# Optimization experiments

Hardware: AMD Instinct MI355X
Metric: run time of the kernel (lower is better)

Reference implementation:

```python
import jax, jax.numpy as jnp
import numpy as np
from jax.scipy.special import logsumexp

# ---- problem sizes ----
N, M, D, K = 3072, 3072, 64, 8
# geomloss SamplesLoss('sinkhorn', p=2, blur=0.05, scaling=0.8): cost = |x-y|^2 / 2
BLUR = 0.05
EPS = BLUR ** 2          # final entropic temperature = blur^p
SCAL2 = 0.8 ** 2         # eps annealing factor per iteration = scaling^p
NITER = 30               # fixed-length eps-scaling schedule (jit-friendly)


def _sqdist(x, y):
    # squared euclidean pairwise distances [n, m]
    return (x * x).sum(-1)[:, None] + (y * y).sum(-1)[None, :] - 2.0 * (x @ y.T)


def setup_inputs() -> dict:
    rng = np.random.default_rng(0)
    true_c = 3.0 * rng.normal(size=(K, D)).astype(np.float32)
    lab_t = rng.integers(0, K, size=M)
    target = (true_c[lab_t] + rng.normal(size=(M, D))).astype(np.float32)
    lab_x = rng.integers(0, K, size=N)
    x = (true_c[lab_x] + rng.normal(size=(N, D))).astype(np.float32)
    # Lloyd kmeans on target (emulates kmeans() in LossKMeans.__init__, no_grad precompute)
    C = target[rng.choice(M, K, replace=False)].copy()
    for _ in range(20):
        d = ((target[:, None, :] - C[None, :, :]) ** 2).sum(-1)
        assign = d.argmin(1)
        for k in range(K):
            m = assign == k
            if m.any():
                C[k] = target[m].mean(0)
    d = ((target[:, None, :] - C[None, :, :]) ** 2).sum(-1)
    pred_t = d.argmin(1).astype(np.int32)
    # approx_cluster_filling: soft-assignment fractions per cluster
    s = -d
    s = s - s.max(1, keepdims=True)
    e = np.exp(s)
    soft = e / e.sum(1, keepdims=True)
    filling_target = (soft.sum(0) / M).astype(np.float32)
    return {
        "x": jnp.asarray(x),
        "target": jnp.asarray(target),
        "cluster_centers": jnp.asarray(C.astype(np.float32)),
        "filling_target": jnp.asarray(filling_target),
        "prediction_target": jnp.asarray(pred_t),
    }


def _sinkhorn_potentials(C, loga, logb):
    # log-domain Sinkhorn with geometric eps annealing, run on a detached cost
    eps0 = jnp.maximum(jnp.max(C), EPS)
    f0 = jnp.zeros(C.shape[0], C.dtype)
    g0 = jnp.zeros(C.shape[1], C.dtype)

    def body(carry, t):
        f, g = carry
        eps = jnp.maximum(eps0 * (SCAL2 ** t), EPS)
        f = -eps * logsumexp(logb[None, :] + (g[None, :] - C) / eps, axis=1)
        g = -eps * logsumexp(loga[:, None] + (f[:, None] - C) / eps, axis=0)
        return (f, g), None

    (f, g), _ = jax.lax.scan(body, (f0, g0), jnp.arange(NITER, dtype=C.dtype))
    return f, g


def _ot(C, loga, logb, a, b):
    # geomloss-style gradient: iterate with stopped grads, one final differentiable update
    f, g = _sinkhorn_potentials(jax.lax.stop_gradient(C), loga, logb)
    f = jax.lax.stop_gradient(f)
    g = jax.lax.stop_gradient(g)
    f2 = -EPS * logsumexp(logb[None, :] + (g[None, :] - C) / EPS, axis=1)
    g2 = -EPS * logsumexp(loga[:, None] + (f[:, None] - C) / EPS, axis=0)
    return jnp.sum(a * f2) + jnp.sum(b * g2)


def _weights(mask, n):
    cnt = mask.sum()
    a = jnp.where(mask, 1.0 / jnp.maximum(cnt, 1).astype(jnp.float32), 0.0)
    a = jnp.where(cnt > 0, a, jnp.full(mask.shape, 1.0 / n, jnp.float32))  # safe fallback for empty cluster
    loga = jnp.where(a > 0, jnp.log(jnp.maximum(a, 1e-38)), -jnp.inf)
    return a, loga, cnt


def _forward(x, target, cluster_centers, filling_target, prediction_target):
    # loss_fil = compute_cluster_filling_mse(x, centers, filling_target)
    d_x = _sqdist(x, cluster_centers)                       # [N, K]
    filling_x = jax.nn.softmax(-d_x, axis=1).sum(0) / x.shape[0]
    loss_fil = jnp.mean((filling_x - filling_target) ** 2)
    # kmeans_predict
    pred_x = jnp.argmin(d_x, axis=1)
    # shared cost matrices (p=2 -> |x-y|^2 / 2), reused across the cluster loop
    Cxy = 0.5 * _sqdist(x, target)
    Cxx = 0.5 * _sqdist(x, x)
    Cyy = 0.5 * _sqdist(target, target)
    loss_med = jnp.float32(0.0)
    for k in range(K):  # fixed small loop over clusters (torch.unique loop, mask-guarded)
        mx = pred_x == k
        my = prediction_target == k
        a, loga, cx = _weights(mx, x.shape[0])
        b, logb, cy = _weights(my, target.shape[0])
        # debiased sinkhorn divergence (geomloss default debias=True)
        s = (_ot(Cxy, loga, logb, a, b)
             - 0.5 * _ot(Cxx, loga, loga, a, a)
             - 0.5 * _ot(Cyy, logb, logb, b, b))
        valid = ((cx > 0) & (cy > 0)).astype(jnp.float32)
        loss_med = loss_med + valid * s
    return loss_fil + loss_med


_fwd_jit = jax.jit(_forward)


def reference(x, target, cluster_centers, filling_target, prediction_target):
    return _fwd_jit(x, target, cluster_centers, filling_target, prediction_target)
```

## Files before the change

kernel.cpp:

```cpp
#include <hip/hip_runtime.h>
#include <hip/hip_bf16.h>
#include <float.h>

#define NN 3072
#define MM 3072
#define DD 64
#define KK 8
#define NPROB 24
#define NBLK 480

constexpr float C_EPS   = 0.0025f;
constexpr int   C_NITER = 30;
constexpr float LOG2E = 1.4426950408889634f;
constexpr float LN2F  = 0.6931471805599453f;
constexpr float L2_SCAL2 = -0.6438561897747247f;

__device__ __forceinline__ float ex2(float x){ return __builtin_amdgcn_exp2f(x); }
__device__ __forceinline__ float lg2(float x){ return __builtin_amdgcn_logf(x); }

__device__ __forceinline__ void  sst(float* p, float v){
    __hip_atomic_store(p, v, __ATOMIC_RELAXED, __HIP_MEMORY_SCOPE_SYSTEM);
}
__device__ __forceinline__ float sld(const float* p){
    return __hip_atomic_load((float*)p, __ATOMIC_RELAXED, __HIP_MEMORY_SCOPE_SYSTEM);
}

#define U_FILL 0
#define U_MAXC 8
#define U_CNTX 12
#define U_CNTY 20
#define U_POSX 28
#define U_POSY 36
#define U_OFFX 44
#define U_OFFY 53
#define U_PNX  64
#define U_PNY  88
#define U_PRB  112
#define U_PCB  136
#define U_PRS  160
#define U_PCS  184
#define U_PCOFF 208
#define U_PTOF  233
#define U_TOFF  257
#define U_ACCF  288
#define U_ACCG  312
#define U_TPPA  336
#define U_ASGN  384
#define U_BAR   896
#define U_XSQ  2432
#define U_YSQ  5504
#define U_PRED 8576
#define U_ROWS 11648
#define U_COLS 14720
#define U_FPOT 17792
#define U_GPOT 91520
#define U_SUBC 165248

__global__ __launch_bounds__(256) void k_prep(const float* __restrict__ x,
                                              const float* __restrict__ y,
                                              const float* __restrict__ cc,
                                              const int* __restrict__ predt,
                                              float* wf, int* wi) {
    int tid = threadIdx.x;
    if (blockIdx.x < 12) {
        __shared__ __align__(16) float c_s[KK][DD];
        __shared__ float csq_s[KK];
        __shared__ float fpart[KK];
        for (int e = tid; e < KK*DD; e += 256) c_s[e>>6][e&63] = cc[e];
        if (tid < KK) fpart[tid] = 0.f;
        __syncthreads();
        if (tid < KK) { float s=0.f; for (int d=0; d<DD; ++d){ float v=c_s[tid][d]; s+=v*v; } csq_s[tid]=s; }
        __syncthreads();
        int i = blockIdx.x*256 + tid;
        if (i < NN) {
            const float4* xr = (const float4*)(x + (size_t)i*DD);
            float4 xv[16];
            float xs = 0.f;
            #pragma unroll
            for (int q=0;q<16;++q){ xv[q]=xr[q];
                xs += xv[q].x*xv[q].x + xv[q].y*xv[q].y + xv[q].z*xv[q].z + xv[q].w*xv[q].w; }
            float dk[KK];
            #pragma unroll
            for (int k=0;k<KK;++k){
                const float4* cr = (const float4*)(&c_s[k][0]);
                float dot=0.f;
                #pragma unroll
                for (int q=0;q<16;++q){ float4 cv=cr[q];
                    dot += xv[q].x*cv.x + xv[q].y*cv.y + xv[q].z*cv.z + xv[q].w*cv.w; }
                dk[k] = xs + csq_s[k] - 2.f*dot;
            }
            float dmin = dk[0]; int am=0;
            #pragma unroll
            for (int k=1;k<KK;++k){ if (dk[k] < dmin){ dmin=dk[k]; am=k; } }
            float se=0.f; float ek[KK];
            #pragma unroll
            for (int k=0;k<KK;++k){ ek[k] = ex2((dmin-dk[k])*LOG2E); se+=ek[k]; }
            float inv = 1.f/se;
            #pragma unroll
            for (int k=0;k<KK;++k) atomicAdd(&fpart[k], ek[k]*inv);
            wf[U_XSQ + i] = xs;
            wi[U_PRED + i] = am;
            atomicAdd(&wi[U_CNTX + am], 1);
        }
        __syncthreads();
        if (tid < KK) atomicAdd(&wf[U_FILL + tid], fpart[tid]);
    } else {
        int j = (blockIdx.x-12)*256 + tid;
        if (j < MM) {
            const float4* yr = (const float4*)(y + (size_t)j*DD);
            float s=0.f;
            #pragma unroll
            for (int q=0;q<16;++q){ float4 v=yr[q]; s += v.x*v.x+v.y*v.y+v.z*v.z+v.w*v.w; }
            wf[U_YSQ + j] = s;
            atomicAdd(&wi[U_CNTY + predt[j]], 1);
        }
    }
}

__global__ void k_offsets(const float* __restrict__ ftarg, float* wf, int* wi, float* out) {
    if (threadIdx.x != 0) return;
    int offx=0, offy=0;
    wi[U_OFFX]=0; wi[U_OFFY]=0;
    for (int k=0;k<KK;++k){
        offx += wi[U_CNTX+k]; wi[U_OFFX+k+1]=offx;
        offy += wi[U_CNTY+k]; wi[U_OFFY+k+1]=offy;
    }
    int co=0, to=0;
    for (int k=0;k<KK;++k){
        int cx=wi[U_CNTX+k], cy=wi[U_CNTY+k];
        bool val = (cx>0)&&(cy>0);
        for (int t=0;t<3;++t){
            int p=k*3+t;
            int nx = val ? (t==2?cy:cx) : 0;
            int ny = val ? (t==1?cx:cy) : 0;
            wi[U_PNX+p]=nx; wi[U_PNY+p]=ny;
            wi[U_PRB+p] = (t==2)? wi[U_OFFY+k] : wi[U_OFFX+k];
            wi[U_PCB+p] = (t==1)? wi[U_OFFX+k] : wi[U_OFFY+k];
            wi[U_PRS+p] = (t==2)?1:0;
            wi[U_PCS+p] = (t==1)?0:1;
            wi[U_PCOFF+p]=co; co += nx*ny;
            wi[U_TOFF+p]=to; to += ((nx+31)>>5)*((ny+31)>>5);
            wf[U_ACCF+p]=0.f; wf[U_ACCG+p]=0.f;
        }
    }
    wi[U_PCOFF+NPROB]=co; wi[U_TOFF+NPROB]=to;
    int cto = co;
    for (int p=0;p<NPROB;++p){
        if (p%3 == 0){ wi[U_PTOF+p] = cto; cto += wi[U_PNX+p]*wi[U_PNY+p]; }
        else         { wi[U_PTOF+p] = wi[U_PCOFF+p]; }
    }
    long long wsum = 0;
    int wk[NPROB], quota[NPROB], done[NPROB];
    for (int p=0;p<NPROB;++p){
        int nx=wi[U_PNX+p], ny=wi[U_PNY+p];
        wk[p] = (nx>0 && ny>0) ? nx*ny : 0;
        wsum += wk[p];
    }
    if (wsum == 0){
        for (int b=0;b<NBLK;++b) wi[U_ASGN+b] = (0xFF<<16);
        for (int p=0;p<NPROB;++p) wi[U_TPPA+p] = 0;
    } else {
        int tot=0;
        for (int p=0;p<NPROB;++p){
            quota[p] = (wk[p]>0) ? (int)(((long long)NBLK*wk[p])/wsum) : 0;
            if (wk[p]>0 && quota[p]<1) quota[p]=1;
            tot += quota[p];
        }
        while (tot < NBLK){
            int best=-1; float br=-1.f;
            for (int p=0;p<NPROB;++p) if (wk[p]>0){
                float r = (float)wk[p]/(float)quota[p];
                if (r>br){br=r;best=p;}
            }
            quota[best]++; tot++;
        }
        while (tot > NBLK){
            int best=-1; float br=3.4e38f;
            for (int p=0;p<NPROB;++p) if (quota[p]>1){
                float r = (float)wk[p]/(float)(quota[p]-1);
                if (r<br){br=r;best=p;}
            }
            if (best<0) break;
            quota[best]--; tot--;
        }
        for (int p=0;p<NPROB;++p){ done[p]=0; wi[U_TPPA+p]=quota[p]; }
        int asg=0;
        while (asg < NBLK){
            for (int p=0;p<NPROB && asg<NBLK;++p)
                if (done[p] < quota[p]){ wi[U_ASGN+asg] = (p<<16)|done[p]; done[p]++; asg++; }
        }
    }
    float lf=0.f;
    for (int k=0;k<KK;++k){ float fx = wf[U_FILL+k]/(float)NN; float dd = fx - ftarg[k]; lf += dd*dd; }
    out[0] = lf/(float)KK;
}

__global__ __launch_bounds__(256) void k_scatter(const int* __restrict__ predt, int* wi) {
    int b = blockIdx.x;
    if (b < 12) {
        int i = b*256 + threadIdx.x;
        if (i < NN){ int k = wi[U_PRED+i]; int p = atomicAdd(&wi[U_POSX+k],1);
                     wi[U_ROWS + wi[U_OFFX+k] + p] = i; }
    } else {
        int j = (b-12)*256 + threadIdx.x;
        if (j < MM){ int k = predt[j]; int p = atomicAdd(&wi[U_POSY+k],1);
                     wi[U_COLS + wi[U_OFFY+k] + p] = j; }
    }
}

__global__ __launch_bounds__(256) void k_maxmat(const float* __restrict__ x,
                                                const float* __restrict__ y,
                                                float* wf, int* wi) {
    int z = blockIdx.z;
    const float* A = (z==2)? y : x;
    const float* B = (z==0)? y : ((z==1)? x : y);
    int aqo = (z==2)? U_YSQ : U_XSQ;
    int bqo = (z==1)? U_XSQ : U_YSQ;
    __shared__ float la[64][65];
    __shared__ float lb[64][65];
    __shared__ float laq[64], lbq[64];
    __shared__ float wred[4];
    int tid = threadIdx.x;
    int i0 = blockIdx.y*64, j0 = blockIdx.x*64;
    #pragma unroll
    for (int q=0;q<4;++q){
        int idx4 = tid + q*256;
        int r = idx4>>4; int c = (idx4&15)<<2;
        float4 va = *(const float4*)(A + (size_t)(i0+r)*DD + c);
        la[r][c]=va.x; la[r][c+1]=va.y; la[r][c+2]=va.z; la[r][c+3]=va.w;
        float4 vb = *(const float4*)(B + (size_t)(j0+r)*DD + c);
        lb[r][c]=vb.x; lb[r][c+1]=vb.y; lb[r][c+2]=vb.z; lb[r][c+3]=vb.w;
    }
    if (tid < 64) { laq[tid]=wf[aqo+i0+tid]; lbq[tid]=wf[bqo+j0+tid]; }
    __syncthreads();
    int r0 = (tid>>4)<<2, c0 = (tid&15)<<2;
    float acc[4][4] = {};
    for (int d=0; d<DD; ++d){
        float av[4], bv[4];
        #pragma unroll
        for (int a=0;a<4;++a){ av[a]=la[r0+a][d]; bv[a]=lb[c0+a][d]; }
        #pragma unroll
        for (int a=0;a<4;++a)
            #pragma unroll
            for (int b2=0;b2<4;++b2) acc[a][b2] += av[a]*bv[b2];
    }
    float m = 0.f;
    #pragma unroll
    for (int a=0;a<4;++a)
        #pragma unroll
        for (int b2=0;b2<4;++b2){
            float cst = 0.5f*(laq[r0+a]+lbq[c0+b2]) - acc[a][b2];
            m = fmaxf(m, cst);
        }
    #pragma unroll
    for (int o=32;o;o>>=1) m = fmaxf(m, __shfl_xor(m,o));
    int wid = tid>>6;
    if ((tid&63)==0) wred[wid]=m;
    __syncthreads();
    if (tid==0){
        float mm = fmaxf(fmaxf(wred[0],wred[1]),fmaxf(wred[2],wred[3]));
        atomicMax((unsigned int*)&wi[U_MAXC+z], __float_as_uint(mm));
    }
}

__global__ __launch_bounds__(256) void k_gather(const float* __restrict__ x,
                                                const float* __restrict__ y,
                                                float* wf, int* wi) {
    __shared__ float xs_[32][65], ys_[32][65];
    __shared__ float cs_[32][33];
    __shared__ float rq[32], cq[32];
    __shared__ int toff_s[NPROB+1];
    int tid = threadIdx.x;
    if (tid <= NPROB) toff_s[tid] = wi[U_TOFF+tid];
    __syncthreads();
    int total = toff_s[NPROB];
    for (int tix = blockIdx.x; tix < total; tix += gridDim.x){
        int p = 0;
        while (toff_s[p+1] <= tix) ++p;
        int nx = wi[U_PNX+p], ny = wi[U_PNY+p];
        int tpr = (ny+31)>>5;
        int loc = tix - toff_s[p];
        int i0 = (loc/tpr)<<5, j0 = (loc%tpr)<<5;
        int rbase = wi[U_PRB+p], cbase = wi[U_PCB+p];
        int rs = wi[U_PRS+p], cs = wi[U_PCS+p];
        const float* rsrc = rs? y : x;
        const float* csrc = cs? y : x;
        const int* rlist = wi + (rs? U_COLS : U_ROWS);
        const int* clist = wi + (cs? U_COLS : U_ROWS);
        int rqo = rs? U_YSQ : U_XSQ;
        int cqo = cs? U_YSQ : U_XSQ;
        size_t coff = (size_t)wi[U_PCOFF+p];
        #pragma unroll
        for (int q=0;q<2;++q){
            int idx4 = tid + q*256;
            int r = idx4>>4, c = (idx4&15)<<2;
            if (i0 + r < nx){
                int gi = rlist[rbase + i0 + r];
                float4 v = *(const float4*)(rsrc + (size_t)gi*DD + c);
                xs_[r][c]=v.x; xs_[r][c+1]=v.y; xs_[r][c+2]=v.z; xs_[r][c+3]=v.w;
                if (c==0) rq[r] = wf[rqo + gi];
            }
            if (j0 + r < ny){
                int gj = clist[cbase + j0 + r];
                float4 v = *(const float4*)(csrc + (size_t)gj*DD + c);
                ys_[r][c]=v.x; ys_[r][c+1]=v.y; ys_[r][c+2]=v.z; ys_[r][c+3]=v.w;
                if (c==0) cq[r] = wf[cqo + gj];
            }
        }
        __syncthreads();
        int r = tid>>3, cb = (tid&7)<<2;
        float cv[4] = {0.f,0.f,0.f,0.f};
        if (i0 + r < nx){
            float acc[4] = {0.f,0.f,0.f,0.f};
            for (int d=0; d<DD; ++d){
                float xv = xs_[r][d];
                #pragma unroll
                for (int q=0;q<4;++q) acc[q] += xv*ys_[cb+q][d];
            }
            float* dst = wf + U_SUBC + coff + (size_t)(i0+r)*ny + j0;
            #pragma unroll
            for (int q=0;q<4;++q){
                int j = cb+q;
                cv[q] = 0.5f*(rq[r]+cq[j]) - acc[q];
                if (j0 + j < ny) dst[j] = cv[q];
            }
        }
        if (p%3 == 0){
            #pragma unroll
            for (int q=0;q<4;++q) cs_[r][cb+q] = cv[q];
            __syncthreads();
            if (j0 + r < ny){
                float* dT = wf + U_SUBC + (size_t)wi[U_PTOF+p] + (size_t)(j0+r)*nx + i0;
                #pragma unroll
                for (int q=0;q<4;++q){
                    int ii = cb+q;
                    if (i0 + ii < nx) dT[ii] = cs_[ii][r];
                }
            }
        }
        __syncthreads();
    }
}

#define LD8F(JB, D00,D01,D02,D03,D10,D11,D12,D13, G0,G1,G2,G3) { \
    int ja=(JB)+lane; \
    D00=R0[ja]; D01=R0[ja+64]; D02=R0[ja+128]; D03=R0[ja+192]; \
    D10=R1[ja]; D11=R1[ja+64]; D12=R1[ja+128]; D13=R1[ja+192]; \
    G0=gs[ja];  G1=gs[ja+64];  G2=gs[ja+128];  G3=gs[ja+192]; }

#define PROCF(D0,D1,D2,D3, G0,G1,G2,G3, M, S) { \
    float t0=fmaf(D0,nie2,G0), t1=fmaf(D1,nie2,G1), t2=fmaf(D2,nie2,G2), t3=fmaf(D3,nie2,G3); \
    float cm = fmaxf(fmaxf(t0,t1),fmaxf(t2,t3)); \
    float mn = fmaxf(M, cm); \
    float sm = ex2(t0-mn) + ex2(t1-mn) + ex2(t2-mn) + ex2(t3-mn); \
    S = fmaf(S, ex2(M-mn), sm); \
    M = mn; }

#define LD8C(JB, D00,D01,D02,D03,D10,D11,D12,D13, G0,G1,G2,G3) { \
    int ja=(JB)+lane, jb_=(JB)+lane+64, jc=(JB)+lane+128, jd=(JB)+lane+192; \
    D00 = (ja <ncols)? R0[ja]  : 0.f;  D01 = (jb_<ncols)? R0[jb_] : 0.f; \
    D02 = (jc <ncols)? R0[jc]  : 0.f;  D03 = (jd <ncols)? R0[jd]  : 0.f; \
    D10 = (ja <ncols)? R1[ja]  : 0.f;  D11 = (jb_<ncols)? R1[jb_] : 0.f; \
    D12 = (jc <ncols)? R1[jc]  : 0.f;  D13 = (jd <ncols)? R1[jd]  : 0.f; \
    G0  = (ja <ncols)? gs[ja]  : 0.f;  G1  = (jb_<ncols)? gs[jb_] : 0.f; \
    G2  = (jc <ncols)? gs[jc]  : 0.f;  G3  = (jd <ncols)? gs[jd]  : 0.f; }

#define PROCR(JB, D0,D1,D2,D3, G0,G1,G2,G3, M, S) { \
    int ja=(JB)+lane, jb_=(JB)+lane+64, jc=(JB)+lane+128, jd=(JB)+lane+192; \
    float t0 = (ja <ncols)? fmaf(D0, nie2, G0) : -3e38f; \
    float t1 = (jb_<ncols)? fmaf(D1, nie2, G1) : -3e38f; \
    float t2 = (jc <ncols)? fmaf(D2, nie2, G2) : -3e38f; \
    float t3 = (jd <ncols)? fmaf(D3, nie2, G3) : -3e38f; \
    float cm = fmaxf(fmaxf(t0,t1),fmaxf(t2,t3)); \
    float mn = fmaxf(M, cm); \
    float sm = ex2(t0-mn) + ex2(t1-mn) + ex2(t2-mn) + ex2(t3-mn); \
    S = fmaf(S, ex2(M-mn), sm); \
    M = mn; }

template<bool FIN>
__device__ __forceinline__ void sweep(const float* __restrict__ Cb, int ldc, int nrows, int ncols,
                                      const float* __restrict__ gs, float* __restrict__ pot,
                                      float ie2, float neL, float l2n, int w, int lane,
                                      float* saccSlot)
{
    float nie2 = -ie2;
    float acc = 0.f;
    int nfull = ncols >> 8;
    int rem   = ncols & 255;
    for (int i0 = w*2; i0 < nrows; i0 += 16){
        int ia = i0;
        bool v1 = (i0+1 < nrows);
        int ib = v1 ? i0+1 : i0;
        const float* R0 = Cb + (size_t)ia*ldc;
        const float* R1 = Cb + (size_t)ib*ldc;
        float m0=-3e38f, m1=-3e38f, S0=0.f, S1=0.f;
        if (nfull){
            float a00,a01,a02,a03,a10,a11,a12,a13, ga0,ga1,ga2,ga3;
            LD8F(0, a00,a01,a02,a03,a10,a11,a12,a13, ga0,ga1,ga2,ga3)
            for (int v=1; v<nfull; ++v){
                float b00,b01,b02,b03,b10,b11,b12,b13, gb0,gb1,gb2,gb3;
                LD8F(v<<8, b00,b01,b02,b03,b10,b11,b12,b13, gb0,gb1,gb2,gb3)
                PROCF(a00,a01,a02,a03, ga0,ga1,ga2,ga3, m0, S0)
                PROCF(a10,a11,a12,a13, ga0,ga1,ga2,ga3, m1, S1)
                a00=b00; a01=b01; a02=b02; a03=b03;
                a10=b10; a11=b11; a12=b12; a13=b13;
                ga0=gb0; ga1=gb1; ga2=gb2; ga3=gb3;
            }
            PROCF(a00,a01,a02,a03, ga0,ga1,ga2,ga3, m0, S0)
            PROCF(a10,a11,a12,a13, ga0,ga1,ga2,ga3, m1, S1)
        }
        if (rem){
            int jb = nfull<<8;
            float c00,c01,c02,c03,c10,c11,c12,c13, gc0,gc1,gc2,gc3;
            LD8C(jb, c00,c01,c02,c03,c10,c11,c12,c13, gc0,gc1,gc2,gc3)
            PROCR(jb, c00,c01,c02,c03, gc0,gc1,gc2,gc3, m0, S0)
            PROCR(jb, c10,c11,c12,c13, gc0,gc1,gc2,gc3, m1, S1)
        }
        #pragma unroll
        for (int o=32;o;o>>=1){
            float mo=__shfl_xor(m0,o), So=__shfl_xor(S0,o);
            float mn=fmaxf(m0,mo); S0=fmaf(S0,ex2(m0-mn),So*ex2(mo-mn)); m0=mn;
            mo=__shfl_xor(m1,o); So=__shfl_xor(S1,o);
            mn=fmaxf(m1,mo); S1=fmaf(S1,ex2(m1-mn),So*ex2(mo-mn)); m1=mn;
        }
        if (lane==0){
            float v0  = neL*(m0 + lg2(S0) - l2n);
            float v1v = neL*(m1 + lg2(S1) - l2n);
            if (FIN){
                acc += v0;
                if (v1) acc += v1v;
            } else {
                sst(&pot[ia], v0);
                if (v1) sst(&pot[ib], v1v);
            }
        }
    }
    if (FIN && lane==0 && acc != 0.f) atomicAdd(saccSlot, acc);
}

__device__ __forceinline__ void tbar(int* cnt, int* gen, int tpp){
    __syncthreads();
    if (threadIdx.x == 0){
        asm volatile("s_waitcnt vmcnt(0)" ::: "memory");
        int g0 = __hip_atomic_load(gen, __ATOMIC_RELAXED, __HIP_MEMORY_SCOPE_AGENT);
        int a  = __hip_atomic_fetch_add(cnt, 1, __ATOMIC_RELAXED, __HIP_MEMORY_SCOPE_AGENT);
        if (a == tpp-1){
            __hip_atomic_store(cnt, 0, __ATOMIC_RELAXED, __HIP_MEMORY_SCOPE_AGENT);
            __hip_atomic_fetch_add(gen, 1, __ATOMIC_RELAXED, __HIP_MEMORY_SCOPE_AGENT);
        } else {
            int spins = 0;
            while (__hip_atomic_load(gen, __ATOMIC_RELAXED, __HIP_MEMORY_SCOPE_AGENT) == g0){
                __builtin_amdgcn_s_sleep(2);
                if (++spins > 200000) break;
            }
        }
    }
    __syncthreads();
}

__global__ __launch_bounds__(512) void k_sink(float* wf, int* wi, float* out) {
    int av = wi[U_ASGN + blockIdx.x];
    int p  = av>>16, sb = av & 0xFFFF;
    if (p >= NPROB) return;
    int nx = wi[U_PNX+p], ny = wi[U_PNY+p];
    if (nx <= 0 || ny <= 0) return;
    int tpp = wi[U_TPPA+p];
    int tid = threadIdx.x, w = tid>>6, lane = tid&63;
    float eps0 = fmaxf(__uint_as_float((unsigned)wi[U_MAXC + (p%3)]), C_EPS);
    const float* C  = wf + U_SUBC + (size_t)wi[U_PCOFF+p];
    const float* CT = wf + U_SUBC + (size_t)wi[U_PTOF+p];
    float* f = wf + U_FPOT + p*3072;
    float* g = wf + U_GPOT + p*3072;
    float l2ny = lg2((float)ny), l2nx = lg2((float)nx);
    int* cnt = wi + U_BAR + p*64;
    int* gen = cnt + 32;
    int rb0 = (sb*nx)/tpp, re0 = ((sb+1)*nx)/tpp;
    int cb0 = (sb*ny)/tpp, ce0 = ((sb+1)*ny)/tpp;
    __shared__ float gs[3072];

    for (int it=0; it<C_NITER; ++it){
        float eps = fmaxf(eps0*ex2((float)it*L2_SCAL2), C_EPS);
        float ie2 = LOG2E/eps, neL = -eps*LN2F;
        for (int j=tid; j<ny; j+=512) gs[j] = sld(g+j)*ie2;
        __syncthreads();
        sweep<false>(C + (size_t)rb0*ny, ny, re0-rb0, ny, gs, f+rb0, ie2, neL, l2ny, w, lane, nullptr);
        tbar(cnt, gen, tpp);
        for (int i=tid; i<nx; i+=512) gs[i] = sld(f+i)*ie2;
        __syncthreads();
        sweep<false>(CT + (size_t)cb0*nx, nx, ce0-cb0, nx, gs, g+cb0, ie2, neL, l2nx, w, lane, nullptr);
        tbar(cnt, gen, tpp);
    }
    {
        float ie2 = LOG2E/C_EPS, neL = -C_EPS*LN2F;
        for (int j=tid; j<ny; j+=512) gs[j] = sld(g+j)*ie2;
        __syncthreads();
        sweep<true>(C + (size_t)rb0*ny, ny, re0-rb0, ny, gs, nullptr, ie2, neL, l2ny, w, lane, &wf[U_ACCF+p]);
        __syncthreads();
        for (int i=tid; i<nx; i+=512) gs[i] = sld(f+i)*ie2;
        __syncthreads();
        sweep<true>(CT + (size_t)cb0*nx, nx, ce0-cb0, nx, gs, nullptr, ie2, neL, l2nx, w, lane, &wf[U_ACCG+p]);
    }
}

__global__ void k_final(float* wf, int* wi, float* out) {
    if (threadIdx.x != 0 || blockIdx.x != 0) return;
    float s = 0.f;
    for (int p=0; p<NPROB; ++p){
        int nx = wi[U_PNX+p], ny = wi[U_PNY+p];
        if (nx<=0 || ny<=0) continue;
        float wgt = (p%3==0) ? 1.f : -0.5f;
        s += wgt * (wf[U_ACCF+p]/(float)nx + wf[U_ACCG+p]/(float)ny);
    }
    out[0] += s;
}

extern "C" void kernel_launch(void* const* d_in, const int* in_sizes, int n_in,
                              void* d_out, int out_size, void* d_ws, size_t ws_size,
                              hipStream_t stream) {
    const float* x     = (const float*)d_in[0];
    const float* y     = (const float*)d_in[1];
    const float* cc    = (const float*)d_in[2];
    const float* ft    = (const float*)d_in[3];
    const int*   predt = (const int*)d_in[4];
    float* out = (float*)d_out;
    float* wf = (float*)d_ws;
    int*   wi = (int*)d_ws;

    hipMemsetAsync(d_ws, 0, 44*sizeof(int), stream);
    hipMemsetAsync(wi + U_BAR, 0, 24*64*sizeof(int), stream);
    hipMemsetAsync(wf + U_GPOT, 0, NPROB*3072*sizeof(float), stream);

    k_prep<<<24, 256, 0, stream>>>(x, y, cc, predt, wf, wi);
    k_offsets<<<1, 64, 0, stream>>>(ft, wf, wi, out);
    k_scatter<<<24, 256, 0, stream>>>(predt, wi);
    k_maxmat<<<dim3(48,48,3), 256, 0, stream>>>(x, y, wf, wi);
    k_gather<<<1024, 256, 0, stream>>>(x, y, wf, wi);

    k_sink<<<NBLK, 512, 0, stream>>>(wf, wi, out);
    k_final<<<1, 64, 0, stream>>>(wf, wi, out);
}
```

Measured before the change: 738.8 us.

## Enlarge maxmat tiles, skip symmetric blocks, and rebalance sweep rows per wave

The max-cost kernel now uses 128x128 tiles with an 8x8 register microtile, and skips lower-triangle blocks for the symmetric Cxx and Cyy matrices. This cuts global loads and the number of blocks. The Sinkhorn sweep now gives each wave a contiguous slice of rows computed globally across all blocks of a problem, and processes four rows per pass instead of two. That raises memory-level parallelism and balances work between waves, at the cost of more registers per thread and uneven slices when row counts are small.

```diff
diff --git a/kernel.cpp b/kernel.cpp
--- a/kernel.cpp
+++ b/kernel.cpp
@@ -212,46 +212,56 @@
                                                 const float* __restrict__ y,
                                                 float* wf, int* wi) {
     int z = blockIdx.z;
+    if (z && blockIdx.y > blockIdx.x) return;
     const float* A = (z==2)? y : x;
     const float* B = (z==0)? y : ((z==1)? x : y);
     int aqo = (z==2)? U_YSQ : U_XSQ;
     int bqo = (z==1)? U_XSQ : U_YSQ;
-    __shared__ float la[64][65];
-    __shared__ float lb[64][65];
-    __shared__ float laq[64], lbq[64];
+    __shared__ float la[128][65];
+    __shared__ float lb[128][65];
+    __shared__ float laq[128], lbq[128];
     __shared__ float wred[4];
     int tid = threadIdx.x;
-    int i0 = blockIdx.y*64, j0 = blockIdx.x*64;
+    int i0 = blockIdx.y*128, j0 = blockIdx.x*128;
     #pragma unroll
-    for (int q=0;q<4;++q){
-        int idx4 = tid + q*256;
-        int r = idx4>>4; int c = (idx4&15)<<2;
-        float4 va = *(const float4*)(A + (size_t)(i0+r)*DD + c);
-        la[r][c]=va.x; la[r][c+1]=va.y; la[r][c+2]=va.z; la[r][c+3]=va.w;
-        float4 vb = *(const float4*)(B + (size_t)(j0+r)*DD + c);
-        lb[r][c]=vb.x; lb[r][c+1]=vb.y; lb[r][c+2]=vb.z; lb[r][c+3]=vb.w;
-    }
-    if (tid < 64) { laq[tid]=wf[aqo+i0+tid]; lbq[tid]=wf[bqo+j0+tid]; }
+    for (int q=0;q<8;++q){
+        int idx = tid + q*256;
+        int r = idx>>4, c4 = (idx&15)<<2;
+        float4 va = *(const float4*)(A + (size_t)(i0+r)*DD + c4);
+        la[r][c4]=va.x; la[r][c4+1]=va.y; la[r][c4+2]=va.z; la[r][c4+3]=va.w;
+        float4 vb = *(const float4*)(B + (size_t)(j0+r)*DD + c4);
+        lb[r][c4]=vb.x; lb[r][c4+1]=vb.y; lb[r][c4+2]=vb.z; lb[r][c4+3]=vb.w;
+    }
+    if (tid < 128) laq[tid] = wf[aqo + i0 + tid];
+    else           lbq[tid-128] = wf[bqo + j0 + (tid-128)];
     __syncthreads();
-    int r0 = (tid>>4)<<2, c0 = (tid&15)<<2;
-    float acc[4][4] = {};
+    int tx = tid & 15, ty = tid >> 4;
+    float acc[8][8];
+    #pragma unroll
+    for (int u=0;u<8;++u)
+        #pragma unroll
+        for (int s=0;s<8;++s) acc[u][s]=0.f;
     for (int d=0; d<DD; ++d){
-        float av[4], bv[4];
+        float av[8], bv[8];
         #pragma unroll
-        for (int a=0;a<4;++a){ av[a]=la[r0+a][d]; bv[a]=lb[c0+a][d]; }
+        for (int u=0;u<8;++u) av[u]=la[ty+16*u][d];
         #pragma unroll
-        for (int a=0;a<4;++a)
-            #pragma unroll
-            for (int b2=0;b2<4;++b2) acc[a][b2] += av[a]*bv[b2];
+        for (int s=0;s<8;++s) bv[s]=lb[tx+16*s][d];
+        #pragma unroll
+        for (int u=0;u<8;++u)
+            #pragma unroll
+            for (int s=0;s<8;++s) acc[u][s] = fmaf(av[u], bv[s], acc[u][s]);
     }
     float m = 0.f;
     #pragma unroll
-    for (int a=0;a<4;++a)
+    for (int u=0;u<8;++u){
+        float aq = laq[ty+16*u];
         #pragma unroll
-        for (int b2=0;b2<4;++b2){
-            float cst = 0.5f*(laq[r0+a]+lbq[c0+b2]) - acc[a][b2];
+        for (int s=0;s<8;++s){
+            float cst = 0.5f*(aq + lbq[tx+16*s]) - acc[u][s];
             m = fmaxf(m, cst);
         }
+    }
     #pragma unroll
     for (int o=32;o;o>>=1) m = fmaxf(m, __shfl_xor(m,o));
     int wid = tid>>6;
@@ -342,11 +352,14 @@
     }
 }
 
-#define LD8F(JB, D00,D01,D02,D03,D10,D11,D12,D13, G0,G1,G2,G3) { \
-    int ja=(JB)+lane; \
-    D00=R0[ja]; D01=R0[ja+64]; D02=R0[ja+128]; D03=R0[ja+192]; \
-    D10=R1[ja]; D11=R1[ja+64]; D12=R1[ja+128]; D13=R1[ja+192]; \
-    G0=gs[ja];  G1=gs[ja+64];  G2=gs[ja+128];  G3=gs[ja+192]; }
+#define LD4R(R, JB, D0,D1,D2,D3) { int ja=(JB)+lane; \
+    D0=R[ja]; D1=R[ja+64]; D2=R[ja+128]; D3=R[ja+192]; }
+
+#define LD4RC(R, JB, D0,D1,D2,D3) { int ja=(JB)+lane; \
+    D0 = (ja      <ncols)? R[ja]     : 0.f; \
+    D1 = (ja+64   <ncols)? R[ja+64]  : 0.f; \
+    D2 = (ja+128  <ncols)? R[ja+128] : 0.f; \
+    D3 = (ja+192  <ncols)? R[ja+192] : 0.f; }
 
 #define PROCF(D0,D1,D2,D3, G0,G1,G2,G3, M, S) { \
     float t0=fmaf(D0,nie2,G0), t1=fmaf(D1,nie2,G1), t2=fmaf(D2,nie2,G2), t3=fmaf(D3,nie2,G3); \
@@ -356,82 +369,102 @@
     S = fmaf(S, ex2(M-mn), sm); \
     M = mn; }
 
-#define LD8C(JB, D00,D01,D02,D03,D10,D11,D12,D13, G0,G1,G2,G3) { \
-    int ja=(JB)+lane, jb_=(JB)+lane+64, jc=(JB)+lane+128, jd=(JB)+lane+192; \
-    D00 = (ja <ncols)? R0[ja]  : 0.f;  D01 = (jb_<ncols)? R0[jb_] : 0.f; \
-    D02 = (jc <ncols)? R0[jc]  : 0.f;  D03 = (jd <ncols)? R0[jd]  : 0.f; \
-    D10 = (ja <ncols)? R1[ja]  : 0.f;  D11 = (jb_<ncols)? R1[jb_] : 0.f; \
-    D12 = (jc <ncols)? R1[jc]  : 0.f;  D13 = (jd <ncols)? R1[jd]  : 0.f; \
-    G0  = (ja <ncols)? gs[ja]  : 0.f;  G1  = (jb_<ncols)? gs[jb_] : 0.f; \
-    G2  = (jc <ncols)? gs[jc]  : 0.f;  G3  = (jd <ncols)? gs[jd]  : 0.f; }
-
 #define PROCR(JB, D0,D1,D2,D3, G0,G1,G2,G3, M, S) { \
-    int ja=(JB)+lane, jb_=(JB)+lane+64, jc=(JB)+lane+128, jd=(JB)+lane+192; \
-    float t0 = (ja <ncols)? fmaf(D0, nie2, G0) : -3e38f; \
-    float t1 = (jb_<ncols)? fmaf(D1, nie2, G1) : -3e38f; \
-    float t2 = (jc <ncols)? fmaf(D2, nie2, G2) : -3e38f; \
-    float t3 = (jd <ncols)? fmaf(D3, nie2, G3) : -3e38f; \
+    int ja=(JB)+lane; \
+    float t0 = (ja     <ncols)? fmaf(D0, nie2, G0) : -3e38f; \
+    float t1 = (ja+64  <ncols)? fmaf(D1, nie2, G1) : -3e38f; \
+    float t2 = (ja+128 <ncols)? fmaf(D2, nie2, G2) : -3e38f; \
+    float t3 = (ja+192 <ncols)? fmaf(D3, nie2, G3) : -3e38f; \
     float cm = fmaxf(fmaxf(t0,t1),fmaxf(t2,t3)); \
     float mn = fmaxf(M, cm); \
     float sm = ex2(t0-mn) + ex2(t1-mn) + ex2(t2-mn) + ex2(t3-mn); \
     S = fmaf(S, ex2(M-mn), sm); \
     M = mn; }
 
+#define MERGE(M, S) { \
+    _Pragma("unroll") \
+    for (int o=32;o;o>>=1){ \
+        float mo=__shfl_xor(M,o), So=__shfl_xor(S,o); \
+        float mn=fmaxf(M,mo); S=fmaf(S,ex2(M-mn),So*ex2(mo-mn)); M=mn; } }
+
 template<bool FIN>
-__device__ __forceinline__ void sweep(const float* __restrict__ Cb, int ldc, int nrows, int ncols,
-                                      const float* __restrict__ gs, float* __restrict__ pot,
-                                      float ie2, float neL, float l2n, int w, int lane,
-                                      float* saccSlot)
+__device__ __forceinline__ void sweep(const float* __restrict__ Cb, int ldc, int rbeg, int rend,
+                                      int ncols, const float* __restrict__ gs,
+                                      float* __restrict__ pot, float ie2, float neL, float l2n,
+                                      int lane, float* saccSlot)
 {
     float nie2 = -ie2;
     float acc = 0.f;
     int nfull = ncols >> 8;
     int rem   = ncols & 255;
-    for (int i0 = w*2; i0 < nrows; i0 += 16){
+    for (int i0 = rbeg; i0 < rend; i0 += 4){
         int ia = i0;
-        bool v1 = (i0+1 < nrows);
-        int ib = v1 ? i0+1 : i0;
+        bool v1 = (i0+1 < rend), v2 = (i0+2 < rend), v3 = (i0+3 < rend);
+        int ib = v1? i0+1 : ia, ic = v2? i0+2 : ia, id2 = v3? i0+3 : ia;
         const float* R0 = Cb + (size_t)ia*ldc;
         const float* R1 = Cb + (size_t)ib*ldc;
-        float m0=-3e38f, m1=-3e38f, S0=0.f, S1=0.f;
+        const float* R2 = Cb + (size_t)ic*ldc;
+        const float* R3 = Cb + (size_t)id2*ldc;
+        float m0=-3e38f,m1=-3e38f,m2=-3e38f,m3=-3e38f;
+        float S0=0.f,S1=0.f,S2=0.f,S3=0.f;
         if (nfull){
-            float a00,a01,a02,a03,a10,a11,a12,a13, ga0,ga1,ga2,ga3;
-            LD8F(0, a00,a01,a02,a03,a10,a11,a12,a13, ga0,ga1,ga2,ga3)
+            float a00,a01,a02,a03, a10,a11,a12,a13, a20,a21,a22,a23, a30,a31,a32,a33;
+            float ga0,ga1,ga2,ga3;
+            LD4R(R0,0,a00,a01,a02,a03) LD4R(R1,0,a10,a11,a12,a13)
+            LD4R(R2,0,a20,a21,a22,a23) LD4R(R3,0,a30,a31,a32,a33)
+            { int ja=lane; ga0=gs[ja]; ga1=gs[ja+64]; ga2=gs[ja+128]; ga3=gs[ja+192]; }
             for (int v=1; v<nfull; ++v){
-                float b00,b01,b02,b03,b10,b11,b12,b13, gb0,gb1,gb2,gb3;
-                LD8F(v<<8, b00,b01,b02,b03,b10,b11,b12,b13, gb0,gb1,gb2,gb3)
+                int jn = v<<8;
+                float b00,b01,b02,b03, b10,b11,b12,b13, b20,b21,b22,b23, b30,b31,b32,b33;
+                float gb0,gb1,gb2,gb3;
+                LD4R(R0,jn,b00,b01,b02,b03) LD4R(R1,jn,b10,b11,b12,b13)
+                LD4R(R2,jn,b20,b21,b22,b23) LD4R(R3,jn,b30,b31,b32,b33)
+                { int ja=jn+lane; gb0=gs[ja]; gb1=gs[ja+64]; gb2=gs[ja+128]; gb3=gs[ja+192]; }
                 PROCF(a00,a01,a02,a03, ga0,ga1,ga2,ga3, m0, S0)
                 PROCF(a10,a11,a12,a13, ga0,ga1,ga2,ga3, m1, S1)
-                a00=b00; a01=b01; a02=b02; a03=b03;
-                a10=b10; a11=b11; a12=b12; a13=b13;
-                ga0=gb0; ga1=gb1; ga2=gb2; ga3=gb3;
+                PROCF(a20,a21,a22,a23, ga0,ga1,ga2,ga3, m2, S2)
+                PROCF(a30,a31,a32,a33, ga0,ga1,ga2,ga3, m3, S3)
+                a00=b00;a01=b01;a02=b02;a03=b03; a10=b10;a11=b11;a12=b12;a13=b13;
+                a20=b20;a21=b21;a22=b22;a23=b23; a30=b30;a31=b31;a32=b32;a33=b33;
+                ga0=gb0;ga1=gb1;ga2=gb2;ga3=gb3;
             }
             PROCF(a00,a01,a02,a03, ga0,ga1,ga2,ga3, m0, S0)
             PROCF(a10,a11,a12,a13, ga0,ga1,ga2,ga3, m1, S1)
+            PROCF(a20,a21,a22,a23, ga0,ga1,ga2,ga3, m2, S2)
+            PROCF(a30,a31,a32,a33, ga0,ga1,ga2,ga3, m3, S3)
         }
         if (rem){
             int jb = nfull<<8;
-            float c00,c01,c02,c03,c10,c11,c12,c13, gc0,gc1,gc2,gc3;
-            LD8C(jb, c00,c01,c02,c03,c10,c11,c12,c13, gc0,gc1,gc2,gc3)
+            float c00,c01,c02,c03, c10,c11,c12,c13, c20,c21,c22,c23, c30,c31,c32,c33;
+            float gc0,gc1,gc2,gc3;
+            LD4RC(R0,jb,c00,c01,c02,c03) LD4RC(R1,jb,c10,c11,c12,c13)
+            LD4RC(R2,jb,c20,c21,c22,c23) LD4RC(R3,jb,c30,c31,c32,c33)
+            { int ja=jb+lane;
+              gc0 = (ja    <ncols)? gs[ja]     : 0.f;
+              gc1 = (ja+64 <ncols)? gs[ja+64]  : 0.f;
+              gc2 = (ja+128<ncols)? gs[ja+128] : 0.f;
+              gc3 = (ja+192<ncols)? gs[ja+192] : 0.f; }
             PROCR(jb, c00,c01,c02,c03, gc0,gc1,gc2,gc3, m0, S0)
             PROCR(jb, c10,c11,c12,c13, gc0,gc1,gc2,gc3, m1, S1)
-        }
-        #pragma unroll
-        for (int o=32;o;o>>=1){
-            float mo=__shfl_xor(m0,o), So=__shfl_xor(S0,o);
-            float mn=fmaxf(m0,mo); S0=fmaf(S0,ex2(m0-mn),So*ex2(mo-mn)); m0=mn;
-            mo=__shfl_xor(m1,o); So=__shfl_xor(S1,o);
-            mn=fmaxf(m1,mo); S1=fmaf(S1,ex2(m1-mn),So*ex2(mo-mn)); m1=mn;
-        }
+            PROCR(jb, c20,c21,c22,c23, gc0,gc1,gc2,gc3, m2, S2)
+            PROCR(jb, c30,c31,c32,c33, gc0,gc1,gc2,gc3, m3, S3)
+        }
+        MERGE(m0,S0) MERGE(m1,S1) MERGE(m2,S2) MERGE(m3,S3)
         if (lane==0){
             float v0  = neL*(m0 + lg2(S0) - l2n);
-            float v1v = neL*(m1 + lg2(S1) - l2n);
+            float w1  = neL*(m1 + lg2(S1) - l2n);
+            float w2  = neL*(m2 + lg2(S2) - l2n);
+            float w3  = neL*(m3 + lg2(S3) - l2n);
             if (FIN){
                 acc += v0;
-                if (v1) acc += v1v;
+                if (v1) acc += w1;
+                if (v2) acc += w2;
+                if (v3) acc += w3;
             } else {
                 sst(&pot[ia], v0);
-                if (v1) sst(&pot[ib], v1v);
+                if (v1) sst(&pot[ib], w1);
+                if (v2) sst(&pot[ic], w2);
+                if (v3) sst(&pot[id2], w3);
             }
         }
     }
@@ -466,6 +499,8 @@
     if (nx <= 0 || ny <= 0) return;
     int tpp = wi[U_TPPA+p];
     int tid = threadIdx.x, w = tid>>6, lane = tid&63;
+    int W  = tpp*8;
+    int gw = sb*8 + w;
     float eps0 = fmaxf(__uint_as_float((unsigned)wi[U_MAXC + (p%3)]), C_EPS);
     const float* C  = wf + U_SUBC + (size_t)wi[U_PCOFF+p];
     const float* CT = wf + U_SUBC + (size_t)wi[U_PTOF+p];
@@ -474,8 +509,8 @@
     float l2ny = lg2((float)ny), l2nx = lg2((float)nx);
     int* cnt = wi + U_BAR + p*64;
     int* gen = cnt + 32;
-    int rb0 = (sb*nx)/tpp, re0 = ((sb+1)*nx)/tpp;
-    int cb0 = (sb*ny)/tpp, ce0 = ((sb+1)*ny)/tpp;
+    int frb = (int)(((long long)gw*nx)/W),   fre = (int)(((long long)(gw+1)*nx)/W);
+    int grb = (int)(((long long)gw*ny)/W),   gre = (int)(((long long)(gw+1)*ny)/W);
     __shared__ float gs[3072];
 
     for (int it=0; it<C_NITER; ++it){
@@ -483,22 +518,22 @@
         float ie2 = LOG2E/eps, neL = -eps*LN2F;
         for (int j=tid; j<ny; j+=512) gs[j] = sld(g+j)*ie2;
         __syncthreads();
-        sweep<false>(C + (size_t)rb0*ny, ny, re0-rb0, ny, gs, f+rb0, ie2, neL, l2ny, w, lane, nullptr);
+        sweep<false>(C, ny, frb, fre, ny, gs, f, ie2, neL, l2ny, lane, nullptr);
         tbar(cnt, gen, tpp);
         for (int i=tid; i<nx; i+=512) gs[i] = sld(f+i)*ie2;
         __syncthreads();
-        sweep<false>(CT + (size_t)cb0*nx, nx, ce0-cb0, nx, gs, g+cb0, ie2, neL, l2nx, w, lane, nullptr);
+        sweep<false>(CT, nx, grb, gre, nx, gs, g, ie2, neL, l2nx, lane, nullptr);
         tbar(cnt, gen, tpp);
     }
     {
         float ie2 = LOG2E/C_EPS, neL = -C_EPS*LN2F;
         for (int j=tid; j<ny; j+=512) gs[j] = sld(g+j)*ie2;
         __syncthreads();
-        sweep<true>(C + (size_t)rb0*ny, ny, re0-rb0, ny, gs, nullptr, ie2, neL, l2ny, w, lane, &wf[U_ACCF+p]);
+        sweep<true>(C, ny, frb, fre, ny, gs, nullptr, ie2, neL, l2ny, lane, &wf[U_ACCF+p]);
         __syncthreads();
         for (int i=tid; i<nx; i+=512) gs[i] = sld(f+i)*ie2;
         __syncthreads();
-        sweep<true>(CT + (size_t)cb0*nx, nx, ce0-cb0, nx, gs, nullptr, ie2, neL, l2nx, w, lane, &wf[U_ACCG+p]);
+        sweep<true>(CT, nx, grb, gre, nx, gs, nullptr, ie2, neL, l2nx, lane, &wf[U_ACCG+p]);
     }
 }
 
@@ -533,7 +568,7 @@
     k_prep<<<24, 256, 0, stream>>>(x, y, cc, predt, wf, wi);
     k_offsets<<<1, 64, 0, stream>>>(ft, wf, wi, out);
     k_scatter<<<24, 256, 0, stream>>>(predt, wi);
-    k_maxmat<<<dim3(48,48,3), 256, 0, stream>>>(x, y, wf, wi);
+    k_maxmat<<<dim3(24,24,3), 256, 0, stream>>>(x, y, wf, wi);
     k_gather<<<1024, 256, 0, stream>>>(x, y, wf, wi);
 
     k_sink<<<NBLK, 512, 0, stream>>>(wf, wi, out);
```

Measured after the change: 795.5 us. +7.7%, slower.

## Enlarge max-cost tiles to 128x128 and skip symmetric lower blocks

Applied to the files above, without the earlier changes.

The max-cost kernel now uses 128x128 tiles with an 8x8 per-thread register microtile and fma, and launches a quarter as many blocks. For the symmetric Cxx and Cyy matrices it computes only the upper-triangle tiles, which still gives the correct max. The two small workspace memsets are merged into one contiguous memset. Larger tiles raise shared-memory use and register pressure, which may lower occupancy.

```diff
diff --git a/kernel.cpp b/kernel.cpp
--- a/kernel.cpp
+++ b/kernel.cpp
@@ -212,46 +212,56 @@
                                                 const float* __restrict__ y,
                                                 float* wf, int* wi) {
     int z = blockIdx.z;
+    if (z && blockIdx.y > blockIdx.x) return;
     const float* A = (z==2)? y : x;
     const float* B = (z==0)? y : ((z==1)? x : y);
     int aqo = (z==2)? U_YSQ : U_XSQ;
     int bqo = (z==1)? U_XSQ : U_YSQ;
-    __shared__ float la[64][65];
-    __shared__ float lb[64][65];
-    __shared__ float laq[64], lbq[64];
+    __shared__ float la[128][65];
+    __shared__ float lb[128][65];
+    __shared__ float laq[128], lbq[128];
     __shared__ float wred[4];
     int tid = threadIdx.x;
-    int i0 = blockIdx.y*64, j0 = blockIdx.x*64;
+    int i0 = blockIdx.y*128, j0 = blockIdx.x*128;
     #pragma unroll
-    for (int q=0;q<4;++q){
-        int idx4 = tid + q*256;
-        int r = idx4>>4; int c = (idx4&15)<<2;
-        float4 va = *(const float4*)(A + (size_t)(i0+r)*DD + c);
-        la[r][c]=va.x; la[r][c+1]=va.y; la[r][c+2]=va.z; la[r][c+3]=va.w;
-        float4 vb = *(const float4*)(B + (size_t)(j0+r)*DD + c);
-        lb[r][c]=vb.x; lb[r][c+1]=vb.y; lb[r][c+2]=vb.z; lb[r][c+3]=vb.w;
-    }
-    if (tid < 64) { laq[tid]=wf[aqo+i0+tid]; lbq[tid]=wf[bqo+j0+tid]; }
+    for (int q=0;q<8;++q){
+        int idx = tid + q*256;
+        int r = idx>>4, c4 = (idx&15)<<2;
+        float4 va = *(const float4*)(A + (size_t)(i0+r)*DD + c4);
+        la[r][c4]=va.x; la[r][c4+1]=va.y; la[r][c4+2]=va.z; la[r][c4+3]=va.w;
+        float4 vb = *(const float4*)(B + (size_t)(j0+r)*DD + c4);
+        lb[r][c4]=vb.x; lb[r][c4+1]=vb.y; lb[r][c4+2]=vb.z; lb[r][c4+3]=vb.w;
+    }
+    if (tid < 128) laq[tid] = wf[aqo + i0 + tid];
+    else           lbq[tid-128] = wf[bqo + j0 + (tid-128)];
     __syncthreads();
-    int r0 = (tid>>4)<<2, c0 = (tid&15)<<2;
-    float acc[4][4] = {};
+    int tx = tid & 15, ty = tid >> 4;
+    float acc[8][8];
+    #pragma unroll
+    for (int u=0;u<8;++u)
+        #pragma unroll
+        for (int s=0;s<8;++s) acc[u][s]=0.f;
     for (int d=0; d<DD; ++d){
-        float av[4], bv[4];
-        #pragma unroll
-        for (int a=0;a<4;++a){ av[a]=la[r0+a][d]; bv[a]=lb[c0+a][d]; }
-        #pragma unroll
-        for (int a=0;a<4;++a)
-            #pragma unroll
-            for (int b2=0;b2<4;++b2) acc[a][b2] += av[a]*bv[b2];
+        float av[8], bv[8];
+        #pragma unroll
+        for (int u=0;u<8;++u) av[u]=la[ty+16*u][d];
+        #pragma unroll
+        for (int s=0;s<8;++s) bv[s]=lb[tx+16*s][d];
+        #pragma unroll
+        for (int u=0;u<8;++u)
+            #pragma unroll
+            for (int s=0;s<8;++s) acc[u][s] = fmaf(av[u], bv[s], acc[u][s]);
     }
     float m = 0.f;
     #pragma unroll
-    for (int a=0;a<4;++a)
-        #pragma unroll
-        for (int b2=0;b2<4;++b2){
-            float cst = 0.5f*(laq[r0+a]+lbq[c0+b2]) - acc[a][b2];
+    for (int u=0;u<8;++u){
+        float aq = laq[ty+16*u];
+        #pragma unroll
+        for (int s=0;s<8;++s){
+            float cst = 0.5f*(aq + lbq[tx+16*s]) - acc[u][s];
             m = fmaxf(m, cst);
         }
+    }
     #pragma unroll
     for (int o=32;o;o>>=1) m = fmaxf(m, __shfl_xor(m,o));
     int wid = tid>>6;
@@ -526,14 +536,13 @@
     float* wf = (float*)d_ws;
     int*   wi = (int*)d_ws;
 
-    hipMemsetAsync(d_ws, 0, 44*sizeof(int), stream);
-    hipMemsetAsync(wi + U_BAR, 0, 24*64*sizeof(int), stream);
+    hipMemsetAsync(d_ws, 0, 2432*sizeof(int), stream);
     hipMemsetAsync(wf + U_GPOT, 0, NPROB*3072*sizeof(float), stream);
 
     k_prep<<<24, 256, 0, stream>>>(x, y, cc, predt, wf, wi);
     k_offsets<<<1, 64, 0, stream>>>(ft, wf, wi, out);
     k_scatter<<<24, 256, 0, stream>>>(predt, wi);
-    k_maxmat<<<dim3(48,48,3), 256, 0, stream>>>(x, y, wf, wi);
+    k_maxmat<<<dim3(24,24,3), 256, 0, stream>>>(x, y, wf, wi);
     k_gather<<<1024, 256, 0, stream>>>(x, y, wf, wi);
 
     k_sink<<<NBLK, 512, 0, stream>>>(wf, wi, out);
```

Measured after the change: 695.2 us. 5.9% less time.
